# Performance work log

Hardware: AMD Instinct MI355X
Metric: run time of the kernel (lower is better)

The kernel has to match this reference:

```python
import jax, jax.numpy as jnp
import numpy as np

N = 131072; E = 1048576; B = 1024
FIN = 128; H = 128; K = 30; C1 = 16; KERN = 5
D = 3 * H                      # 384 = hidden*num_layers
POOL_LEN = (K - KERN + 1) // 2 # 13
EPS = 1e-5


def setup_inputs() -> dict:
    key = jax.random.key(0)
    ks = jax.random.split(key, 12)
    w = lambda k, shape, s=0.05: (jax.random.normal(k, shape, jnp.float32) * s)
    z = jax.random.randint(ks[0], (N,), 0, FIN, dtype=jnp.int32)
    edge_index = jax.random.randint(ks[1], (2, E), 0, N, dtype=jnp.int32)
    batch = jnp.sort(jax.random.randint(ks[2], (N,), 0, B, dtype=jnp.int32))
    return dict(
        z=z, edge_index=edge_index, batch=batch,
        W0=w(ks[3], (FIN, H)), b0=jnp.zeros((H,), jnp.float32),
        W1=w(ks[4], (H, H)),   b1=jnp.zeros((H,), jnp.float32),
        W2=w(ks[5], (H, H)),   b2=jnp.zeros((H,), jnp.float32),
        Wc1=w(ks[6], (C1, D)), bc1=jnp.zeros((C1,), jnp.float32),
        Wc2=w(ks[7], (2 * C1, C1, KERN)), bc2=jnp.zeros((2 * C1,), jnp.float32),
        g1=jnp.ones((C1,), jnp.float32),  be1=jnp.zeros((C1,), jnp.float32),
        g2=jnp.ones((2 * C1,), jnp.float32), be2=jnp.zeros((2 * C1,), jnp.float32),
        Wl1=w(ks[8], (128, 2 * C1 * POOL_LEN)), bl1=jnp.zeros((128,), jnp.float32),
        Wl2=w(ks[9], (1, 128)), bl2=jnp.zeros((1,), jnp.float32),
        rm1=jnp.zeros((C1,), jnp.float32), rv1=jnp.ones((C1,), jnp.float32),
        rm2=jnp.zeros((2 * C1,), jnp.float32), rv2=jnp.ones((2 * C1,), jnp.float32),
    )


def _bn(h, g, be, rm, rv):
    # eval-mode BatchNorm1d over channel axis 1 of [B, C, L]
    scale = (g * jax.lax.rsqrt(rv + EPS))[None, :, None]
    return (h - rm[None, :, None]) * scale + be[None, :, None]


def _forward(z, edge_index, batch, W0, b0, W1, b1, W2, b2, Wc1, bc1, Wc2, bc2,
             g1, be1, g2, be2, Wl1, bl1, Wl2, bl2, rm1, rv1, rm2, rv2):
    # --- GCN normalization with self-loops (PyG gcn_norm) ---
    loops = jnp.arange(N)
    row = jnp.concatenate([edge_index[0], loops])  # source
    col = jnp.concatenate([edge_index[1], loops])  # target (aggregation)
    deg = jax.ops.segment_sum(jnp.ones(E + N, jnp.float32), col, num_segments=N)
    dis = jax.lax.rsqrt(deg)  # deg >= 1 thanks to self-loops
    norm = dis[row] * dis[col]

    def gcn(x, W, b):
        msg = (x @ W)[row] * norm[:, None]              # [E+N, H]
        return jax.ops.segment_sum(msg, col, num_segments=N) + b

    x = jax.nn.one_hot(z, FIN, dtype=jnp.float32)       # [N, FIN]
    xs = []
    for W, b in ((W0, b0), (W1, b1), (W2, b2)):
        x = jnp.tanh(gcn(x, W, b))
        xs.append(x)
    x = jnp.concatenate(xs, axis=-1)                    # [N, D]

    # --- global_sort_pool: per graph, sort by last channel desc, keep top-k, zero-pad ---
    order = jnp.lexsort((-x[:, -1], batch))             # batch asc, last-channel desc
    xb, bs = x[order], batch[order]
    counts = jax.ops.segment_sum(jnp.ones(N, jnp.int32), batch, num_segments=B)
    starts = jnp.cumsum(counts) - counts
    rank = jnp.arange(N) - starts[bs]                   # within-graph rank
    dest = jnp.where(rank < K, rank, K)                 # overflow bucket at K
    pooled = jnp.zeros((B, K + 1, D), jnp.float32).at[bs, dest].set(xb)[:, :K]  # [B,K,D]

    # --- conv1d_1 (kernel=stride=D) == dense over the D channels of each kept node ---
    h = jnp.einsum('bkd,cd->bck', pooled, Wc1) + bc1[None, :, None]  # [B,C1,K]
    h = _bn(jax.nn.relu(h), g1, be1, rm1, rv1)
    # --- conv1d_2 ---
    h = jax.lax.conv_general_dilated(h, Wc2, (1,), 'VALID',
                                     dimension_numbers=('NCH', 'OIH', 'NCH'))
    h = h + bc2[None, :, None]                          # [B,2C1,K-KERN+1]
    h = _bn(jax.nn.relu(h), g2, be2, rm2, rv2)
    # --- maxpool(2,2), flatten, dense head (dropout is identity in eval) ---
    h = h.reshape(B, 2 * C1, POOL_LEN, 2).max(-1)
    h = jax.nn.relu(h.reshape(B, -1) @ Wl1.T + bl1)
    return (h @ Wl2.T + bl2).reshape(-1)                # [B]


def reference(z, edge_index, batch, W0, b0, W1, b1, W2, b2, Wc1, bc1, Wc2, bc2,
              g1, be1, g2, be2, Wl1, bl1, Wl2, bl2, rm1, rv1, rm2, rv2):
    return _forward(z, edge_index, batch, W0, b0, W1, b1, W2, b2, Wc1, bc1, Wc2, bc2,
                    g1, be1, g2, be2, Wl1, bl1, Wl2, bl2, rm1, rv1, rm2, rv2)
```

## Files before the change

kernel.cpp:

```cpp
#include <hip/hip_runtime.h>
#include <math.h>

constexpr int HD = 128;
constexpr int DD = 384;
constexpr int KK = 30;
constexpr int C1N = 16;
constexpr int C2N = 32;
constexpr int KERN5 = 5;
constexpr int CONVL = 26;
constexpr int PL = 13;
constexpr int FLAT = 416;

__global__ void deg_kernel(const int* __restrict__ col, int* __restrict__ cnt, int E) {
  int e = blockIdx.x * blockDim.x + threadIdx.x;
  if (e < E) atomicAdd(&cnt[col[e]], 1);
}

__global__ void scan1_kernel(const int* __restrict__ cnt, int* __restrict__ bsum, int N) {
  __shared__ int red[256];
  int t = threadIdx.x, b = blockIdx.x;
  int base = b * 1024 + t * 4;
  int s = 0;
#pragma unroll
  for (int j = 0; j < 4; ++j) { int idx = base + j; if (idx < N) s += cnt[idx]; }
  red[t] = s;
  __syncthreads();
  for (int o = 128; o > 0; o >>= 1) { if (t < o) red[t] += red[t + o]; __syncthreads(); }
  if (t == 0) bsum[b] = red[0];
}

__global__ void scan2_kernel(int* __restrict__ bsum, int nb) {
  __shared__ int s[1024];
  int t = threadIdx.x;
  int v = (t < nb) ? bsum[t] : 0;
  s[t] = v;
  __syncthreads();
  for (int o = 1; o < 1024; o <<= 1) {
    int u = (t >= o) ? s[t - o] : 0;
    __syncthreads();
    s[t] += u;
    __syncthreads();
  }
  if (t < nb) bsum[t] = s[t] - v;
}

__global__ void scan3_kernel(const int* __restrict__ cnt, const int* __restrict__ bsum,
                             int* __restrict__ offsets, int N) {
  __shared__ int red[256];
  int t = threadIdx.x, b = blockIdx.x;
  int base = b * 1024 + t * 4;
  int v[4]; int s = 0;
#pragma unroll
  for (int j = 0; j < 4; ++j) { int idx = base + j; v[j] = (idx < N) ? cnt[idx] : 0; s += v[j]; }
  red[t] = s;
  __syncthreads();
  for (int o = 1; o < 256; o <<= 1) {
    int u = (t >= o) ? red[t - o] : 0;
    __syncthreads();
    red[t] += u;
    __syncthreads();
  }
  int run = bsum[b] + red[t] - s;
#pragma unroll
  for (int j = 0; j < 4; ++j) {
    int idx = base + j;
    if (idx < N) {
      offsets[idx] = run;
      run += v[j];
      if (idx == N - 1) offsets[N] = run;
    }
  }
}

__global__ void dis_kernel(const int* __restrict__ cnt, float* __restrict__ dis, int N) {
  int i = blockIdx.x * blockDim.x + threadIdx.x;
  if (i < N) dis[i] = 1.0f / sqrtf((float)(cnt[i] + 1));
}

__global__ void fill_kernel(const int* __restrict__ row, const int* __restrict__ col,
                            const int* __restrict__ offsets, int* __restrict__ cursor,
                            int* __restrict__ csr_src, int E) {
  int e = blockIdx.x * blockDim.x + threadIdx.x;
  if (e < E) {
    int c = col[e];
    int p = offsets[c] + atomicAdd(&cursor[c], 1);
    csr_src[p] = row[e];
  }
}

__global__ __launch_bounds__(256) void agg0_kernel(
    const int* __restrict__ z, const int* __restrict__ offsets,
    const int* __restrict__ csr_src, const float* __restrict__ dis,
    const float* __restrict__ W0, const float* __restrict__ b0,
    float* __restrict__ x1, int N) {
  int wid = (blockIdx.x * blockDim.x + threadIdx.x) >> 6;
  int lane = threadIdx.x & 63;
  if (wid >= N) return;
  int i = wid;
  int c0 = lane * 2;
  float di = dis[i];
  int beg = offsets[i], end = offsets[i + 1];
  float ax = 0.f, ay = 0.f;
  int e = beg;
  for (; e + 8 <= end; e += 8) {
    int s0 = csr_src[e],     s1 = csr_src[e + 1], s2 = csr_src[e + 2], s3 = csr_src[e + 3];
    int s4 = csr_src[e + 4], s5 = csr_src[e + 5], s6 = csr_src[e + 6], s7 = csr_src[e + 7];
    float w0 = dis[s0], w1 = dis[s1], w2 = dis[s2], w3 = dis[s3];
    float w4 = dis[s4], w5 = dis[s5], w6 = dis[s6], w7 = dis[s7];
    const float2 y0 = *(const float2*)(W0 + (size_t)z[s0] * HD + c0);
    const float2 y1 = *(const float2*)(W0 + (size_t)z[s1] * HD + c0);
    const float2 y2 = *(const float2*)(W0 + (size_t)z[s2] * HD + c0);
    const float2 y3 = *(const float2*)(W0 + (size_t)z[s3] * HD + c0);
    const float2 y4 = *(const float2*)(W0 + (size_t)z[s4] * HD + c0);
    const float2 y5 = *(const float2*)(W0 + (size_t)z[s5] * HD + c0);
    const float2 y6 = *(const float2*)(W0 + (size_t)z[s6] * HD + c0);
    const float2 y7 = *(const float2*)(W0 + (size_t)z[s7] * HD + c0);
    float axa = fmaf(w0, y0.x, fmaf(w1, y1.x, fmaf(w2, y2.x, w3 * y3.x)));
    float axb = fmaf(w4, y4.x, fmaf(w5, y5.x, fmaf(w6, y6.x, w7 * y7.x)));
    float aya = fmaf(w0, y0.y, fmaf(w1, y1.y, fmaf(w2, y2.y, w3 * y3.y)));
    float ayb = fmaf(w4, y4.y, fmaf(w5, y5.y, fmaf(w6, y6.y, w7 * y7.y)));
    ax += axa + axb;
    ay += aya + ayb;
  }
  for (; e + 4 <= end; e += 4) {
    int s0 = csr_src[e], s1 = csr_src[e + 1], s2 = csr_src[e + 2], s3 = csr_src[e + 3];
    float w0 = dis[s0], w1 = dis[s1], w2 = dis[s2], w3 = dis[s3];
    const float2 y0 = *(const float2*)(W0 + (size_t)z[s0] * HD + c0);
    const float2 y1 = *(const float2*)(W0 + (size_t)z[s1] * HD + c0);
    const float2 y2 = *(const float2*)(W0 + (size_t)z[s2] * HD + c0);
    const float2 y3 = *(const float2*)(W0 + (size_t)z[s3] * HD + c0);
    ax = fmaf(w0, y0.x, fmaf(w1, y1.x, fmaf(w2, y2.x, fmaf(w3, y3.x, ax))));
    ay = fmaf(w0, y0.y, fmaf(w1, y1.y, fmaf(w2, y2.y, fmaf(w3, y3.y, ay))));
  }
  for (; e < end; ++e) {
    int s = csr_src[e];
    float w = dis[s];
    const float2 ys = *(const float2*)(W0 + (size_t)z[s] * HD + c0);
    ax = fmaf(w, ys.x, ax);
    ay = fmaf(w, ys.y, ay);
  }
  const float2 yi = *(const float2*)(W0 + (size_t)z[i] * HD + c0);
  float inv = di * di;
  float ox = tanhf(di * ax + inv * yi.x + b0[c0]);
  float oy = tanhf(di * ay + inv * yi.y + b0[c0 + 1]);
  *(float2*)(x1 + (size_t)i * HD + c0) = make_float2(ox, oy);
}

__global__ __launch_bounds__(256) void agg_kernel(
    const float* __restrict__ x, const int* __restrict__ offsets,
    const int* __restrict__ csr_src, const float* __restrict__ dis,
    float* __restrict__ T, int N) {
  int hw = (blockIdx.x * blockDim.x + threadIdx.x) >> 5;
  int lane = threadIdx.x & 31;
  if (hw >= N) return;
  int i = hw;
  int c0 = lane * 4;
  float di = dis[i];
  int beg = offsets[i], end = offsets[i + 1];
  float ax = 0.f, ay = 0.f, az = 0.f, aw = 0.f;
  int e = beg;
  for (; e + 8 <= end; e += 8) {
    int s0 = csr_src[e],     s1 = csr_src[e + 1], s2 = csr_src[e + 2], s3 = csr_src[e + 3];
    int s4 = csr_src[e + 4], s5 = csr_src[e + 5], s6 = csr_src[e + 6], s7 = csr_src[e + 7];
    float w0 = dis[s0], w1 = dis[s1], w2 = dis[s2], w3 = dis[s3];
    float w4 = dis[s4], w5 = dis[s5], w6 = dis[s6], w7 = dis[s7];
    const float4 y0 = *(const float4*)(x + (size_t)s0 * HD + c0);
    const float4 y1 = *(const float4*)(x + (size_t)s1 * HD + c0);
    const float4 y2 = *(const float4*)(x + (size_t)s2 * HD + c0);
    const float4 y3 = *(const float4*)(x + (size_t)s3 * HD + c0);
    const float4 y4 = *(const float4*)(x + (size_t)s4 * HD + c0);
    const float4 y5 = *(const float4*)(x + (size_t)s5 * HD + c0);
    const float4 y6 = *(const float4*)(x + (size_t)s6 * HD + c0);
    const float4 y7 = *(const float4*)(x + (size_t)s7 * HD + c0);
    ax = fmaf(w0, y0.x, fmaf(w1, y1.x, fmaf(w2, y2.x, fmaf(w3, y3.x, ax))));
    ay = fmaf(w0, y0.y, fmaf(w1, y1.y, fmaf(w2, y2.y, fmaf(w3, y3.y, ay))));
    az = fmaf(w0, y0.z, fmaf(w1, y1.z, fmaf(w2, y2.z, fmaf(w3, y3.z, az))));
    aw = fmaf(w0, y0.w, fmaf(w1, y1.w, fmaf(w2, y2.w, fmaf(w3, y3.w, aw))));
    ax = fmaf(w4, y4.x, fmaf(w5, y5.x, fmaf(w6, y6.x, fmaf(w7, y7.x, ax))));
    ay = fmaf(w4, y4.y, fmaf(w5, y5.y, fmaf(w6, y6.y, fmaf(w7, y7.y, ay))));
    az = fmaf(w4, y4.z, fmaf(w5, y5.z, fmaf(w6, y6.z, fmaf(w7, y7.z, az))));
    aw = fmaf(w4, y4.w, fmaf(w5, y5.w, fmaf(w6, y6.w, fmaf(w7, y7.w, aw))));
  }
  for (; e + 4 <= end; e += 4) {
    int s0 = csr_src[e], s1 = csr_src[e + 1], s2 = csr_src[e + 2], s3 = csr_src[e + 3];
    float w0 = dis[s0], w1 = dis[s1], w2 = dis[s2], w3 = dis[s3];
    const float4 y0 = *(const float4*)(x + (size_t)s0 * HD + c0);
    const float4 y1 = *(const float4*)(x + (size_t)s1 * HD + c0);
    const float4 y2 = *(const float4*)(x + (size_t)s2 * HD + c0);
    const float4 y3 = *(const float4*)(x + (size_t)s3 * HD + c0);
    ax = fmaf(w0, y0.x, fmaf(w1, y1.x, fmaf(w2, y2.x, fmaf(w3, y3.x, ax))));
    ay = fmaf(w0, y0.y, fmaf(w1, y1.y, fmaf(w2, y2.y, fmaf(w3, y3.y, ay))));
    az = fmaf(w0, y0.z, fmaf(w1, y1.z, fmaf(w2, y2.z, fmaf(w3, y3.z, az))));
    aw = fmaf(w0, y0.w, fmaf(w1, y1.w, fmaf(w2, y2.w, fmaf(w3, y3.w, aw))));
  }
  for (; e < end; ++e) {
    int s = csr_src[e];
    float w = dis[s];
    const float4 ys = *(const float4*)(x + (size_t)s * HD + c0);
    ax = fmaf(w, ys.x, ax);
    ay = fmaf(w, ys.y, ay);
    az = fmaf(w, ys.z, az);
    aw = fmaf(w, ys.w, aw);
  }
  const float4 xi = *(const float4*)(x + (size_t)i * HD + c0);
  float inv = di * di;
  float4 o = make_float4(di * ax + inv * xi.x, di * ay + inv * xi.y,
                         di * az + inv * xi.z, di * aw + inv * xi.w);
  *(float4*)(T + (size_t)i * HD + c0) = o;
}

__global__ __launch_bounds__(256) void gemm_kernel(
    float* __restrict__ T, const float* __restrict__ W, const float* __restrict__ b, int N) {
  __shared__ float Xs[128][33];
  __shared__ float Ws[32][128];
  int t = threadIdx.x;
  int r0 = blockIdx.x * 128;
  int ty = t >> 4, tx = t & 15;
  int R0 = ty * 8;
  float acc[8][8];
#pragma unroll
  for (int a = 0; a < 8; ++a)
#pragma unroll
    for (int c = 0; c < 8; ++c) acc[a][c] = 0.f;

  for (int kb = 0; kb < 128; kb += 32) {
    __syncthreads();
    for (int l = t; l < 1024; l += 256) {
      int r = l >> 3, c4 = (l & 7) << 2;
      float4 v = *(const float4*)(T + (size_t)(r0 + r) * HD + kb + c4);
      Xs[r][c4] = v.x; Xs[r][c4 + 1] = v.y; Xs[r][c4 + 2] = v.z; Xs[r][c4 + 3] = v.w;
    }
    for (int l = t; l < 1024; l += 256) {
      int k = l >> 5, c4 = (l & 31) << 2;
      *(float4*)(&Ws[k][c4]) = *(const float4*)(W + (size_t)(kb + k) * HD + c4);
    }
    __syncthreads();
#pragma unroll
    for (int k = 0; k < 32; ++k) {
      float a[8];
#pragma unroll
      for (int ri = 0; ri < 8; ++ri) a[ri] = Xs[R0 + ri][k];
      float4 blo = *(const float4*)(&Ws[k][tx * 4]);
      float4 bhi = *(const float4*)(&Ws[k][64 + tx * 4]);
      float bb[8] = {blo.x, blo.y, blo.z, blo.w, bhi.x, bhi.y, bhi.z, bhi.w};
#pragma unroll
      for (int ri = 0; ri < 8; ++ri)
#pragma unroll
        for (int ci = 0; ci < 8; ++ci)
          acc[ri][ci] = fmaf(a[ri], bb[ci], acc[ri][ci]);
    }
  }
  float4 bl = *(const float4*)(b + tx * 4);
  float4 bh = *(const float4*)(b + 64 + tx * 4);
#pragma unroll
  for (int ri = 0; ri < 8; ++ri) {
    float4 o0 = make_float4(tanhf(acc[ri][0] + bl.x), tanhf(acc[ri][1] + bl.y),
                            tanhf(acc[ri][2] + bl.z), tanhf(acc[ri][3] + bl.w));
    float4 o1 = make_float4(tanhf(acc[ri][4] + bh.x), tanhf(acc[ri][5] + bh.y),
                            tanhf(acc[ri][6] + bh.z), tanhf(acc[ri][7] + bh.w));
    *(float4*)(T + (size_t)(r0 + R0 + ri) * HD + tx * 4) = o0;
    *(float4*)(T + (size_t)(r0 + R0 + ri) * HD + 64 + tx * 4) = o1;
  }
}

__global__ void gstart_kernel(const int* __restrict__ batch, int* __restrict__ gstart,
                              int N, int B) {
  int g = blockIdx.x * blockDim.x + threadIdx.x;
  if (g > B) return;
  int lo = 0, hi = N;
  while (lo < hi) { int mid = (lo + hi) >> 1; if (batch[mid] < g) lo = mid + 1; else hi = mid; }
  gstart[g] = lo;
}

__global__ __launch_bounds__(512) void head_kernel(
    const float* __restrict__ X1, const float* __restrict__ X2, const float* __restrict__ X3,
    const int* __restrict__ gstart,
    const float* __restrict__ Wc1, const float* __restrict__ bc1,
    const float* __restrict__ Wc2, const float* __restrict__ bc2,
    const float* __restrict__ g1, const float* __restrict__ be1,
    const float* __restrict__ g2, const float* __restrict__ be2,
    const float* __restrict__ rm1, const float* __restrict__ rv1,
    const float* __restrict__ rm2, const float* __restrict__ rv2,
    const float* __restrict__ Wl1, const float* __restrict__ bl1,
    const float* __restrict__ Wl2, const float* __restrict__ bl2,
    float* __restrict__ out) {
  constexpr int MAXC = 512;
  __shared__ float vals[MAXC];
  __shared__ int   sel[KK];
  __shared__ float ph[KK][385];
  __shared__ float h1b[C1N][KK + 1];
  float* h2b  = &ph[0][0];
  float* pp   = &ph[0][0] + 832;
  float* part = &ph[0][0] + 1248;
  float* l1v  = &ph[0][0] + 1760;

  int g = blockIdx.x, t = threadIdx.x;
  int start = gstart[g];
  int count = gstart[g + 1] - start;
  if (count > MAXC) count = MAXC;
  int kk = count < KK ? count : KK;

  for (int i = t; i < count; i += 512)
    vals[i] = X3[(size_t)(start + i) * HD + (HD - 1)];
  __syncthreads();
  if (t < count) {
    float vi = vals[t];
    int rank = 0;
    for (int j = 0; j < count; ++j) {
      float vj = vals[j];
      rank += (vj > vi) || (vj == vi && j < t);
    }
    if (rank < KK) sel[rank] = t;
  }
  __syncthreads();

  for (int l = t; l < KK * DD; l += 512) {
    int r = l / DD, d = l - r * DD;
    float v = 0.f;
    if (r < kk) {
      size_t n = (size_t)(start + sel[r]);
      v = (d < HD) ? X1[n * HD + d]
        : (d < 2 * HD) ? X2[n * HD + (d - HD)]
                       : X3[n * HD + (d - 2 * HD)];
    }
    ph[r][d] = v;
  }
  __syncthreads();

  if (t < C1N * KK) {
    int c = t / KK, k = t - c * KK;
    const float* w = Wc1 + c * DD;
    float s = bc1[c];
    for (int d = 0; d < DD; ++d) s = fmaf(ph[k][d], w[d], s);
    s = fmaxf(s, 0.f);
    float sc = g1[c] * rsqrtf(rv1[c] + 1e-5f);
    h1b[c][k] = (s - rm1[c]) * sc + be1[c];
  }
  __syncthreads();

  for (int l = t; l < C2N * CONVL; l += 512) {
    int o = l / CONVL, tt = l - o * CONVL;
    float s = bc2[o];
    const float* w = Wc2 + o * (C1N * KERN5);
#pragma unroll
    for (int c = 0; c < C1N; ++c)
#pragma unroll
      for (int q = 0; q < KERN5; ++q)
        s = fmaf(h1b[c][tt + q], w[c * KERN5 + q], s);
    s = fmaxf(s, 0.f);
    float sc = g2[o] * rsqrtf(rv2[o] + 1e-5f);
    h2b[o * CONVL + tt] = (s - rm2[o]) * sc + be2[o];
  }
  __syncthreads();

  if (t < FLAT) {
    int o = t / PL, u = t - o * PL;
    pp[t] = fmaxf(h2b[o * CONVL + 2 * u], h2b[o * CONVL + 2 * u + 1]);
  }
  __syncthreads();

  {
    int j = t & 127, h = t >> 7;
    const int Q = FLAT / 4;
    const float* w = Wl1 + (size_t)j * FLAT + h * Q;
    float s = (h == 0) ? bl1[j] : 0.f;
    for (int f = 0; f < Q; ++f) s = fmaf(pp[h * Q + f], w[f], s);
    part[t] = s;
  }
  __syncthreads();
  if (t < 128) l1v[t] = fmaxf(part[t] + part[t + 128] + part[t + 256] + part[t + 384], 0.f);
  __syncthreads();

  if (t < 64) {
    float s = l1v[t] * Wl2[t] + l1v[t + 64] * Wl2[t + 64];
#pragma unroll
    for (int o2 = 32; o2 > 0; o2 >>= 1) s += __shfl_down(s, o2);
    if (t == 0) out[g] = s + bl2[0];
  }
}

extern "C" void kernel_launch(void* const* d_in, const int* in_sizes, int n_in,
                              void* d_out, int out_size, void* d_ws, size_t ws_size,
                              hipStream_t stream) {
  const int*   z    = (const int*)d_in[0];
  const int*   ei   = (const int*)d_in[1];
  const int*   batch= (const int*)d_in[2];
  const float* W0   = (const float*)d_in[3];
  const float* b0   = (const float*)d_in[4];
  const float* W1   = (const float*)d_in[5];
  const float* b1   = (const float*)d_in[6];
  const float* W2   = (const float*)d_in[7];
  const float* b2   = (const float*)d_in[8];
  const float* Wc1  = (const float*)d_in[9];
  const float* bc1  = (const float*)d_in[10];
  const float* Wc2  = (const float*)d_in[11];
  const float* bc2  = (const float*)d_in[12];
  const float* g1   = (const float*)d_in[13];
  const float* be1  = (const float*)d_in[14];
  const float* g2   = (const float*)d_in[15];
  const float* be2  = (const float*)d_in[16];
  const float* Wl1  = (const float*)d_in[17];
  const float* bl1  = (const float*)d_in[18];
  const float* Wl2  = (const float*)d_in[19];
  const float* bl2  = (const float*)d_in[20];
  const float* rm1  = (const float*)d_in[21];
  const float* rv1  = (const float*)d_in[22];
  const float* rm2  = (const float*)d_in[23];
  const float* rv2  = (const float*)d_in[24];

  const int N = in_sizes[0];
  const int E = in_sizes[1] / 2;
  const int B = out_size;
  const int* rowp = ei;
  const int* colp = ei + E;

  char* base = (char*)d_ws;
  size_t off = 0;
  auto alloc = [&](size_t bytes) -> void* {
    void* p = base + off;
    off += (bytes + 255) & ~(size_t)255;
    return p;
  };
  int*   cnt     = (int*)alloc((size_t)N * 4);
  int*   offsets = (int*)alloc(((size_t)N + 1) * 4);
  int*   cursor  = (int*)alloc((size_t)N * 4);
  int*   csr_src = (int*)alloc((size_t)E * 4);
  float* dis     = (float*)alloc((size_t)N * 4);
  int*   gstart  = (int*)alloc(((size_t)B + 1) * 4);
  int*   bsum    = (int*)alloc(1024 * 4);
  float* X1      = (float*)alloc((size_t)N * HD * 4);
  float* X2      = (float*)alloc((size_t)N * HD * 4);
  float* X3      = (float*)alloc((size_t)N * HD * 4);
  (void)ws_size; (void)n_in;

  hipMemsetAsync(cnt, 0, (size_t)N * 4, stream);
  hipMemsetAsync(cursor, 0, (size_t)N * 4, stream);

  const int nb = (N + 1023) / 1024;
  deg_kernel<<<(E + 255) / 256, 256, 0, stream>>>(colp, cnt, E);
  scan1_kernel<<<nb, 256, 0, stream>>>(cnt, bsum, N);
  scan2_kernel<<<1, 1024, 0, stream>>>(bsum, nb);
  scan3_kernel<<<nb, 256, 0, stream>>>(cnt, bsum, offsets, N);
  dis_kernel<<<(N + 255) / 256, 256, 0, stream>>>(cnt, dis, N);
  fill_kernel<<<(E + 255) / 256, 256, 0, stream>>>(rowp, colp, offsets, cursor, csr_src, E);

  agg0_kernel<<<(N + 3) / 4, 256, 0, stream>>>(z, offsets, csr_src, dis, W0, b0, X1, N);
  agg_kernel<<<N / 8, 256, 0, stream>>>(X1, offsets, csr_src, dis, X2, N);
  gemm_kernel<<<N / 128, 256, 0, stream>>>(X2, W1, b1, N);
  agg_kernel<<<N / 8, 256, 0, stream>>>(X2, offsets, csr_src, dis, X3, N);
  gemm_kernel<<<N / 128, 256, 0, stream>>>(X3, W2, b2, N);

  gstart_kernel<<<(B + 1 + 255) / 256, 256, 0, stream>>>(batch, gstart, N, B);
  head_kernel<<<B, 512, 0, stream>>>(X1, X2, X3, gstart, Wc1, bc1, Wc2, bc2, g1, be1, g2, be2,
                                     rm1, rv1, rm2, rv2, Wl1, bl1, Wl2, bl2, (float*)d_out);
}
```

Measured before the change: 726.9 us.

## Fuse dis into scan, use half-wave float4 agg0, and use 512-thread GEMM blocks

Three unrelated changes. The inverse-sqrt degree computation moves into scan3, which removes the separate dis_kernel launch and its extra read of cnt. agg0 now assigns a 32-lane half-wave per node with float4 gathers instead of a full wave with float2, halving the lanes per node and widening each load. The GEMM goes to 512 threads with a 4x8 tile per thread, cutting register pressure to raise occupancy at the cost of less register reuse per shared-memory load.

Measured after the change: 684.6 us. 1.06x faster.

```diff
diff --git a/kernel.cpp b/kernel.cpp
--- a/kernel.cpp
+++ b/kernel.cpp
@@ -45,7 +45,7 @@
 }
 
 __global__ void scan3_kernel(const int* __restrict__ cnt, const int* __restrict__ bsum,
-                             int* __restrict__ offsets, int N) {
+                             int* __restrict__ offsets, float* __restrict__ dis, int N) {
   __shared__ int red[256];
   int t = threadIdx.x, b = blockIdx.x;
   int base = b * 1024 + t * 4;
@@ -67,14 +67,10 @@
     if (idx < N) {
       offsets[idx] = run;
       run += v[j];
+      dis[idx] = 1.0f / sqrtf((float)(v[j] + 1));
       if (idx == N - 1) offsets[N] = run;
     }
   }
-}
-
-__global__ void dis_kernel(const int* __restrict__ cnt, float* __restrict__ dis, int N) {
-  int i = blockIdx.x * blockDim.x + threadIdx.x;
-  if (i < N) dis[i] = 1.0f / sqrtf((float)(cnt[i] + 1));
 }
 
 __global__ void fill_kernel(const int* __restrict__ row, const int* __restrict__ col,
@@ -93,57 +89,66 @@
     const int* __restrict__ csr_src, const float* __restrict__ dis,
     const float* __restrict__ W0, const float* __restrict__ b0,
     float* __restrict__ x1, int N) {
-  int wid = (blockIdx.x * blockDim.x + threadIdx.x) >> 6;
-  int lane = threadIdx.x & 63;
-  if (wid >= N) return;
-  int i = wid;
-  int c0 = lane * 2;
+  int hw = (blockIdx.x * blockDim.x + threadIdx.x) >> 5;
+  int lane = threadIdx.x & 31;
+  if (hw >= N) return;
+  int i = hw;
+  int c0 = lane * 4;
   float di = dis[i];
   int beg = offsets[i], end = offsets[i + 1];
-  float ax = 0.f, ay = 0.f;
+  float ax = 0.f, ay = 0.f, az = 0.f, aw = 0.f;
   int e = beg;
   for (; e + 8 <= end; e += 8) {
     int s0 = csr_src[e],     s1 = csr_src[e + 1], s2 = csr_src[e + 2], s3 = csr_src[e + 3];
     int s4 = csr_src[e + 4], s5 = csr_src[e + 5], s6 = csr_src[e + 6], s7 = csr_src[e + 7];
     float w0 = dis[s0], w1 = dis[s1], w2 = dis[s2], w3 = dis[s3];
     float w4 = dis[s4], w5 = dis[s5], w6 = dis[s6], w7 = dis[s7];
-    const float2 y0 = *(const float2*)(W0 + (size_t)z[s0] * HD + c0);
-    const float2 y1 = *(const float2*)(W0 + (size_t)z[s1] * HD + c0);
-    const float2 y2 = *(const float2*)(W0 + (size_t)z[s2] * HD + c0);
-    const float2 y3 = *(const float2*)(W0 + (size_t)z[s3] * HD + c0);
-    const float2 y4 = *(const float2*)(W0 + (size_t)z[s4] * HD + c0);
-    const float2 y5 = *(const float2*)(W0 + (size_t)z[s5] * HD + c0);
-    const float2 y6 = *(const float2*)(W0 + (size_t)z[s6] * HD + c0);
-    const float2 y7 = *(const float2*)(W0 + (size_t)z[s7] * HD + c0);
-    float axa = fmaf(w0, y0.x, fmaf(w1, y1.x, fmaf(w2, y2.x, w3 * y3.x)));
-    float axb = fmaf(w4, y4.x, fmaf(w5, y5.x, fmaf(w6, y6.x, w7 * y7.x)));
-    float aya = fmaf(w0, y0.y, fmaf(w1, y1.y, fmaf(w2, y2.y, w3 * y3.y)));
-    float ayb = fmaf(w4, y4.y, fmaf(w5, y5.y, fmaf(w6, y6.y, w7 * y7.y)));
-    ax += axa + axb;
-    ay += aya + ayb;
+    const float4 y0 = *(const float4*)(W0 + (size_t)z[s0] * HD + c0);
+    const float4 y1 = *(const float4*)(W0 + (size_t)z[s1] * HD + c0);
+    const float4 y2 = *(const float4*)(W0 + (size_t)z[s2] * HD + c0);
+    const float4 y3 = *(const float4*)(W0 + (size_t)z[s3] * HD + c0);
+    const float4 y4 = *(const float4*)(W0 + (size_t)z[s4] * HD + c0);
+    const float4 y5 = *(const float4*)(W0 + (size_t)z[s5] * HD + c0);
+    const float4 y6 = *(const float4*)(W0 + (size_t)z[s6] * HD + c0);
+    const float4 y7 = *(const float4*)(W0 + (size_t)z[s7] * HD + c0);
+    ax = fmaf(w0, y0.x, fmaf(w1, y1.x, fmaf(w2, y2.x, fmaf(w3, y3.x, ax))));
+    ay = fmaf(w0, y0.y, fmaf(w1, y1.y, fmaf(w2, y2.y, fmaf(w3, y3.y, ay))));
+    az = fmaf(w0, y0.z, fmaf(w1, y1.z, fmaf(w2, y2.z, fmaf(w3, y3.z, az))));
+    aw = fmaf(w0, y0.w, fmaf(w1, y1.w, fmaf(w2, y2.w, fmaf(w3, y3.w, aw))));
+    ax = fmaf(w4, y4.x, fmaf(w5, y5.x, fmaf(w6, y6.x, fmaf(w7, y7.x, ax))));
+    ay = fmaf(w4, y4.y, fmaf(w5, y5.y, fmaf(w6, y6.y, fmaf(w7, y7.y, ay))));
+    az = fmaf(w4, y4.z, fmaf(w5, y5.z, fmaf(w6, y6.z, fmaf(w7, y7.z, az))));
+    aw = fmaf(w4, y4.w, fmaf(w5, y5.w, fmaf(w6, y6.w, fmaf(w7, y7.w, aw))));
   }
   for (; e + 4 <= end; e += 4) {
     int s0 = csr_src[e], s1 = csr_src[e + 1], s2 = csr_src[e + 2], s3 = csr_src[e + 3];
     float w0 = dis[s0], w1 = dis[s1], w2 = dis[s2], w3 = dis[s3];
-    const float2 y0 = *(const float2*)(W0 + (size_t)z[s0] * HD + c0);
-    const float2 y1 = *(const float2*)(W0 + (size_t)z[s1] * HD + c0);
-    const float2 y2 = *(const float2*)(W0 + (size_t)z[s2] * HD + c0);
-    const float2 y3 = *(const float2*)(W0 + (size_t)z[s3] * HD + c0);
+    const float4 y0 = *(const float4*)(W0 + (size_t)z[s0] * HD + c0);
+    const float4 y1 = *(const float4*)(W0 + (size_t)z[s1] * HD + c0);
+    const float4 y2 = *(const float4*)(W0 + (size_t)z[s2] * HD + c0);
+    const float4 y3 = *(const float4*)(W0 + (size_t)z[s3] * HD + c0);
     ax = fmaf(w0, y0.x, fmaf(w1, y1.x, fmaf(w2, y2.x, fmaf(w3, y3.x, ax))));
     ay = fmaf(w0, y0.y, fmaf(w1, y1.y, fmaf(w2, y2.y, fmaf(w3, y3.y, ay))));
+    az = fmaf(w0, y0.z, fmaf(w1, y1.z, fmaf(w2, y2.z, fmaf(w3, y3.z, az))));
+    aw = fmaf(w0, y0.w, fmaf(w1, y1.w, fmaf(w2, y2.w, fmaf(w3, y3.w, aw))));
   }
   for (; e < end; ++e) {
     int s = csr_src[e];
     float w = dis[s];
-    const float2 ys = *(const float2*)(W0 + (size_t)z[s] * HD + c0);
+    const float4 ys = *(const float4*)(W0 + (size_t)z[s] * HD + c0);
     ax = fmaf(w, ys.x, ax);
     ay = fmaf(w, ys.y, ay);
-  }
-  const float2 yi = *(const float2*)(W0 + (size_t)z[i] * HD + c0);
+    az = fmaf(w, ys.z, az);
+    aw = fmaf(w, ys.w, aw);
+  }
+  const float4 yi = *(const float4*)(W0 + (size_t)z[i] * HD + c0);
+  const float4 bb = *(const float4*)(b0 + c0);
   float inv = di * di;
-  float ox = tanhf(di * ax + inv * yi.x + b0[c0]);
-  float oy = tanhf(di * ay + inv * yi.y + b0[c0 + 1]);
-  *(float2*)(x1 + (size_t)i * HD + c0) = make_float2(ox, oy);
+  float4 o = make_float4(tanhf(di * ax + inv * yi.x + bb.x),
+                         tanhf(di * ay + inv * yi.y + bb.y),
+                         tanhf(di * az + inv * yi.z + bb.z),
+                         tanhf(di * aw + inv * yi.w + bb.w));
+  *(float4*)(x1 + (size_t)i * HD + c0) = o;
 }
 
 __global__ __launch_bounds__(256) void agg_kernel(
@@ -209,42 +214,42 @@
   *(float4*)(T + (size_t)i * HD + c0) = o;
 }
 
-__global__ __launch_bounds__(256) void gemm_kernel(
+__global__ __launch_bounds__(512) void gemm_kernel(
     float* __restrict__ T, const float* __restrict__ W, const float* __restrict__ b, int N) {
   __shared__ float Xs[128][33];
   __shared__ float Ws[32][128];
   int t = threadIdx.x;
   int r0 = blockIdx.x * 128;
   int ty = t >> 4, tx = t & 15;
-  int R0 = ty * 8;
-  float acc[8][8];
-#pragma unroll
-  for (int a = 0; a < 8; ++a)
+  int R0 = ty * 4;
+  float acc[4][8];
+#pragma unroll
+  for (int a = 0; a < 4; ++a)
 #pragma unroll
     for (int c = 0; c < 8; ++c) acc[a][c] = 0.f;
 
   for (int kb = 0; kb < 128; kb += 32) {
     __syncthreads();
-    for (int l = t; l < 1024; l += 256) {
+    for (int l = t; l < 1024; l += 512) {
       int r = l >> 3, c4 = (l & 7) << 2;
       float4 v = *(const float4*)(T + (size_t)(r0 + r) * HD + kb + c4);
       Xs[r][c4] = v.x; Xs[r][c4 + 1] = v.y; Xs[r][c4 + 2] = v.z; Xs[r][c4 + 3] = v.w;
     }
-    for (int l = t; l < 1024; l += 256) {
+    for (int l = t; l < 1024; l += 512) {
       int k = l >> 5, c4 = (l & 31) << 2;
       *(float4*)(&Ws[k][c4]) = *(const float4*)(W + (size_t)(kb + k) * HD + c4);
     }
     __syncthreads();
 #pragma unroll
     for (int k = 0; k < 32; ++k) {
-      float a[8];
-#pragma unroll
-      for (int ri = 0; ri < 8; ++ri) a[ri] = Xs[R0 + ri][k];
+      float a[4];
+#pragma unroll
+      for (int ri = 0; ri < 4; ++ri) a[ri] = Xs[R0 + ri][k];
       float4 blo = *(const float4*)(&Ws[k][tx * 4]);
       float4 bhi = *(const float4*)(&Ws[k][64 + tx * 4]);
       float bb[8] = {blo.x, blo.y, blo.z, blo.w, bhi.x, bhi.y, bhi.z, bhi.w};
 #pragma unroll
-      for (int ri = 0; ri < 8; ++ri)
+      for (int ri = 0; ri < 4; ++ri)
 #pragma unroll
         for (int ci = 0; ci < 8; ++ci)
           acc[ri][ci] = fmaf(a[ri], bb[ci], acc[ri][ci]);
@@ -253,7 +258,7 @@
   float4 bl = *(const float4*)(b + tx * 4);
   float4 bh = *(const float4*)(b + 64 + tx * 4);
 #pragma unroll
-  for (int ri = 0; ri < 8; ++ri) {
+  for (int ri = 0; ri < 4; ++ri) {
     float4 o0 = make_float4(tanhf(acc[ri][0] + bl.x), tanhf(acc[ri][1] + bl.y),
                             tanhf(acc[ri][2] + bl.z), tanhf(acc[ri][3] + bl.w));
     float4 o1 = make_float4(tanhf(acc[ri][4] + bh.x), tanhf(acc[ri][5] + bh.y),
@@ -440,15 +445,14 @@
   deg_kernel<<<(E + 255) / 256, 256, 0, stream>>>(colp, cnt, E);
   scan1_kernel<<<nb, 256, 0, stream>>>(cnt, bsum, N);
   scan2_kernel<<<1, 1024, 0, stream>>>(bsum, nb);
-  scan3_kernel<<<nb, 256, 0, stream>>>(cnt, bsum, offsets, N);
-  dis_kernel<<<(N + 255) / 256, 256, 0, stream>>>(cnt, dis, N);
+  scan3_kernel<<<nb, 256, 0, stream>>>(cnt, bsum, offsets, dis, N);
   fill_kernel<<<(E + 255) / 256, 256, 0, stream>>>(rowp, colp, offsets, cursor, csr_src, E);
 
-  agg0_kernel<<<(N + 3) / 4, 256, 0, stream>>>(z, offsets, csr_src, dis, W0, b0, X1, N);
+  agg0_kernel<<<N / 8, 256, 0, stream>>>(z, offsets, csr_src, dis, W0, b0, X1, N);
   agg_kernel<<<N / 8, 256, 0, stream>>>(X1, offsets, csr_src, dis, X2, N);
-  gemm_kernel<<<N / 128, 256, 0, stream>>>(X2, W1, b1, N);
+  gemm_kernel<<<N / 128, 512, 0, stream>>>(X2, W1, b1, N);
   agg_kernel<<<N / 8, 256, 0, stream>>>(X2, offsets, csr_src, dis, X3, N);
-  gemm_kernel<<<N / 128, 256, 0, stream>>>(X3, W2, b2, N);
+  gemm_kernel<<<N / 128, 512, 0, stream>>>(X3, W2, b2, N);
 
   gstart_kernel<<<(B + 1 + 255) / 256, 256, 0, stream>>>(batch, gstart, N, B);
   head_kernel<<<B, 512, 0, stream>>>(X1, X2, X3, gstart, Wc1, bc1, Wc2, bc2, g1, be1, g2, be2,
```
